# Kernel tuning notes

Hardware: AMD Instinct MI355X
Metric: run time of the kernel (lower is better)

## Reference

```python
import jax, jax.numpy as jnp
import numpy as np

N_NODES = 100000
N_EDGES = 3200000
N_GRAPHS = 512


def setup_inputs() -> dict:
    key = jax.random.key(0)
    k1, k2, k3, k4, k5 = jax.random.split(key, 5)
    x = jax.random.normal(k1, (N_NODES, 5), dtype=jnp.float32)
    edge_index = jax.random.randint(k2, (2, N_EDGES), 0, N_NODES, dtype=jnp.int64)
    batch = jnp.sort(jax.random.randint(k3, (N_NODES,), 0, N_GRAPHS, dtype=jnp.int64))
    W1 = jax.random.normal(k4, (5, 16), dtype=jnp.float32) * (1.0 / np.sqrt(5.0))
    b1 = jnp.zeros((16,), dtype=jnp.float32)
    W2 = jax.random.normal(k5, (16, 16), dtype=jnp.float32) * 0.25
    b2 = jnp.zeros((16,), dtype=jnp.float32)
    return {"x": x, "edge_index": edge_index, "batch": batch,
            "W1": W1, "b1": b1, "W2": W2, "b2": b2}


def _gcn_conv(x, src, dst, norm, W, b, n_nodes):
    # PyG GCNConv: h = X W; out_i = sum_{j->i} norm_ij * h_j + b
    h = x @ W                                   # [N, out]
    msgs = h[src] * norm[:, None]               # gather + scale  [E_tot, out]
    out = jax.ops.segment_sum(msgs, dst, num_segments=n_nodes)
    return out + b


def reference(x, edge_index, batch, W1, b1, W2, b2):
    n = x.shape[0]
    # add self-loops (GCNConv default)
    loops = jnp.arange(n, dtype=edge_index.dtype)
    src = jnp.concatenate([edge_index[0], loops])
    dst = jnp.concatenate([edge_index[1], loops])
    # symmetric normalization: deg computed on destination nodes
    deg = jax.ops.segment_sum(jnp.ones_like(src, dtype=x.dtype), dst, num_segments=n)
    dinv = jnp.where(deg > 0, jax.lax.rsqrt(deg), 0.0)
    norm = dinv[src] * dinv[dst]                # [E_tot]

    h = jax.nn.relu(_gcn_conv(x, src, dst, norm, W1, b1, n))
    h = jax.nn.relu(_gcn_conv(h, src, dst, norm, W2, b2, n))

    # global mean pool over graphs in the batch
    sums = jax.ops.segment_sum(h, batch, num_segments=N_GRAPHS)
    cnts = jax.ops.segment_sum(jnp.ones((n,), dtype=h.dtype), batch, num_segments=N_GRAPHS)
    return sums / jnp.maximum(cnts, 1.0)[:, None]
```

## Files before the change

kernel.cpp:

```cpp
#include <hip/hip_runtime.h>

#define N_NODES  100000
#define N_EDGES  3200000
#define N_GRAPHS 512
#define F_IN     5
#define F_HID    16

#define PBLK   512
#define CHUNK  8192
#define NCHUNK ((N_EDGES + CHUNK - 1) / CHUNK)
#define BKT_NODES 256
#define NBKT ((N_NODES + BKT_NODES - 1) / BKT_NODES)
#define CAP 10240


__device__ inline unsigned short f2bf(float f) {
    unsigned u = __float_as_uint(f);
    return (unsigned short)((u + 0x7fffu + ((u >> 16) & 1u)) >> 16);
}
__device__ inline float bf2f(unsigned short h) {
    return __uint_as_float(((unsigned)h) << 16);
}
__device__ inline float4 cvt4(ushort4 u) {
    return make_float4(bf2f(u.x), bf2f(u.y), bf2f(u.z), bf2f(u.w));
}
__device__ inline float4 shfl_xor4(float4 v, int m) {
    return make_float4(__shfl_xor(v.x, m, 64), __shfl_xor(v.y, m, 64),
                       __shfl_xor(v.z, m, 64), __shfl_xor(v.w, m, 64));
}

template <int NW>
__device__ inline int block_incl_scan(int v, int t, int* wsum) {
    int lane = t & 63, wave = t >> 6;
    int x = v;
#pragma unroll
    for (int o = 1; o < 64; o <<= 1) {
        int y = __shfl_up(x, o, 64);
        if (lane >= o) x += y;
    }
    if (lane == 63) wsum[wave] = x;
    __syncthreads();
    if (t < 64) {
        int w = (t < NW) ? wsum[t] : 0;
#pragma unroll
        for (int o = 1; o < NW; o <<= 1) {
            int y = __shfl_up(w, o, 64);
            if (t >= o) w += y;
        }
        if (t < NW) wsum[t] = w;
    }
    __syncthreads();
    return x + (wave ? wsum[wave - 1] : 0);
}

__device__ inline float4 row_gather(const ushort4* __restrict__ pb4, int i, int j,
                                    int beg, int end, const int* __restrict__ col) {
    float4 acc = cvt4(pb4[i * 4 + j]);
    int k = beg;
    for (; k + 3 < end; k += 4) {
        int s0 = col[k], s1 = col[k + 1], s2 = col[k + 2], s3 = col[k + 3];
        ushort4 a = pb4[s0 * 4 + j];
        ushort4 b = pb4[s1 * 4 + j];
        ushort4 c = pb4[s2 * 4 + j];
        ushort4 d = pb4[s3 * 4 + j];
        float4 fa = cvt4(a), fb = cvt4(b), fc = cvt4(c), fd = cvt4(d);
        acc.x += fa.x + fb.x + fc.x + fd.x;
        acc.y += fa.y + fb.y + fc.y + fd.y;
        acc.z += fa.z + fb.z + fc.z + fd.z;
        acc.w += fa.w + fb.w + fc.w + fd.w;
    }
    for (; k < end; k++) {
        float4 f = cvt4(pb4[col[k] * 4 + j]);
        acc.x += f.x; acc.y += f.y; acc.z += f.z; acc.w += f.w;
    }
    return acc;
}


__global__ void k_zero(int* __restrict__ cursor, float* __restrict__ out,
                       float* __restrict__ cnt) {
    int i = blockIdx.x * blockDim.x + threadIdx.x;
    if (i < NBKT) cursor[i] = 0;
    if (i < N_GRAPHS * F_HID) out[i] = 0.0f;
    if (i < N_GRAPHS) cnt[i] = 0.0f;
}

__global__ __launch_bounds__(PBLK) void k_part(const int* __restrict__ src,
                                               const int* __restrict__ dst,
                                               int* __restrict__ cursor,
                                               unsigned* __restrict__ packed) {
    __shared__ int hist[PBLK];
    __shared__ int scn[PBLK];
    __shared__ int rnk[PBLK];
    __shared__ int gbase[PBLK];
    __shared__ int wsum[8];
    int t = threadIdx.x;
    int chunk0 = blockIdx.x * CHUNK;
    int n = min(CHUNK, N_EDGES - chunk0);
    hist[t] = 0;
    __syncthreads();
    int ls[CHUNK / PBLK], ld[CHUNK / PBLK];
    for (int k = t, idx = 0; k < n; k += PBLK, idx++) {
        ls[idx] = src[chunk0 + k];
        ld[idx] = dst[chunk0 + k];
        atomicAdd(&hist[ld[idx] >> 8], 1);
    }
    __syncthreads();
    int v = hist[t];
    int incl = block_incl_scan<8>(v, t, wsum);
    int excl = incl - v;
    scn[t] = excl;
    rnk[t] = excl;
    gbase[t] = (v > 0) ? atomicAdd(&cursor[t], v) : 0;
    __syncthreads();
    for (int k = t, idx = 0; k < n; k += PBLK, idx++) {
        int d = ld[idx], s = ls[idx];
        int b = d >> 8;
        int r = atomicAdd(&rnk[b], 1);
        int g = gbase[b] + (r - scn[b]);
        if (g < CAP)
            packed[(size_t)b * CAP + g] = ((unsigned)s << 8) | (unsigned)(d & 255);
    }
}

__global__ __launch_bounds__(512) void k_scanb(const int* __restrict__ cursor,
                                               int* __restrict__ bktBase) {
    __shared__ int wsum[8];
    int t = threadIdx.x;
    int v = (t < NBKT) ? min(cursor[t], CAP) : 0;
    int incl = block_incl_scan<8>(v, t, wsum);
    if (t < NBKT) bktBase[t] = incl - v;
    if (t == NBKT - 1) bktBase[NBKT] = incl;
}

__global__ __launch_bounds__(512) void k_csr(const int* __restrict__ cursor,
                                             const int* __restrict__ bktBase,
                                             const unsigned* __restrict__ packed,
                                             const float* __restrict__ x,
                                             const float* __restrict__ W1,
                                             int* __restrict__ row_ptr,
                                             int* __restrict__ col,
                                             float* __restrict__ dinv,
                                             unsigned short* __restrict__ pb) {
    __shared__ int hist[BKT_NODES];
    __shared__ int rnk[BKT_NODES];
    __shared__ int wsum[8];
    __shared__ float w1[F_IN * F_HID];
    int b = blockIdx.x, t = threadIdx.x;
    int n = min(cursor[b], CAP);
    int base = bktBase[b];
    if (t < BKT_NODES) hist[t] = 0;
    if (t >= 512 - F_IN * F_HID) w1[t - (512 - F_IN * F_HID)] = W1[t - (512 - F_IN * F_HID)];
    __syncthreads();
    const unsigned* pk = packed + (size_t)b * CAP;
    for (int k = t; k < n; k += 512)
        atomicAdd(&hist[pk[k] & 255], 1);
    __syncthreads();
    int v = (t < BKT_NODES) ? hist[t] : 0;
    int incl = block_incl_scan<8>(v, t, wsum);
    int excl = incl - v;
    if (t < BKT_NODES) rnk[t] = excl;
    __syncthreads();
    for (int k = t; k < n; k += 512) {
        unsigned w = pk[k];
        int r = atomicAdd(&rnk[w & 255], 1);
        col[base + r] = (int)(w >> 8);
    }
    if (t < BKT_NODES) {
        int node = b * BKT_NODES + t;
        if (node < N_NODES) {
            row_ptr[node] = base + excl;
            float di = rsqrtf((float)(1 + v));
            dinv[node] = di;
            if (node == N_NODES - 1) row_ptr[N_NODES] = base + excl + v;
            float xi[F_IN];
#pragma unroll
            for (int k = 0; k < F_IN; k++) xi[k] = x[node * F_IN + k];
            float hv[F_HID];
#pragma unroll
            for (int c = 0; c < F_HID; c++) {
                float h = 0.0f;
#pragma unroll
                for (int k = 0; k < F_IN; k++) h += xi[k] * w1[k * F_HID + c];
                hv[c] = h * di;
            }
            unsigned pkk[8];
#pragma unroll
            for (int q = 0; q < 8; q++)
                pkk[q] = (unsigned)f2bf(hv[2 * q]) | ((unsigned)f2bf(hv[2 * q + 1]) << 16);
            uint4* d4 = (uint4*)(pb + (size_t)node * F_HID);
            d4[0] = make_uint4(pkk[0], pkk[1], pkk[2], pkk[3]);
            d4[1] = make_uint4(pkk[4], pkk[5], pkk[6], pkk[7]);
        }
    }
}

__global__ __launch_bounds__(256) void k_pull_mid(const int* __restrict__ row_ptr,
                                                  const int* __restrict__ col,
                                                  const unsigned short* __restrict__ pb,
                                                  const float* __restrict__ dinv,
                                                  const float* __restrict__ W2,
                                                  const float* __restrict__ b1,
                                                  unsigned short* __restrict__ pb2) {
    __shared__ float w[F_HID * F_HID];
    __shared__ float bb[F_HID];
    int t = threadIdx.x;
    w[t] = W2[t];
    if (t < F_HID) bb[t] = b1[t];
    __syncthreads();
    int gid = blockIdx.x * 256 + t;
    int i = gid >> 2;
    int j = gid & 3;
    if (i >= N_NODES) return;
    int beg = row_ptr[i], end = row_ptr[i + 1];
    float4 acc = row_gather((const ushort4*)pb, i, j, beg, end, col);
    float di = dinv[i];
    float4 mine;
    mine.x = fmaxf(di * acc.x + bb[4 * j + 0], 0.0f);
    mine.y = fmaxf(di * acc.y + bb[4 * j + 1], 0.0f);
    mine.z = fmaxf(di * acc.z + bb[4 * j + 2], 0.0f);
    mine.w = fmaxf(di * acc.w + bb[4 * j + 3], 0.0f);
    float4 o1 = shfl_xor4(mine, 1);
    float4 o2 = shfl_xor4(mine, 2);
    float4 o3 = shfl_xor4(mine, 3);
    float4 hq0 = (j == 0) ? mine : ((j == 1) ? o1 : ((j == 2) ? o2 : o3));
    float4 hq1 = (j == 1) ? mine : ((j == 0) ? o1 : ((j == 3) ? o2 : o3));
    float4 hq2 = (j == 2) ? mine : ((j == 3) ? o1 : ((j == 0) ? o2 : o3));
    float4 hq3 = (j == 3) ? mine : ((j == 2) ? o1 : ((j == 1) ? o2 : o3));
    float hc[F_HID] = {hq0.x, hq0.y, hq0.z, hq0.w, hq1.x, hq1.y, hq1.z, hq1.w,
                       hq2.x, hq2.y, hq2.z, hq2.w, hq3.x, hq3.y, hq3.z, hq3.w};
    float m0 = 0.0f, m1 = 0.0f, m2 = 0.0f, m3 = 0.0f;
#pragma unroll
    for (int c = 0; c < F_HID; c++) {
        float4 wv = *(const float4*)&w[c * F_HID + 4 * j];
        float hv = hc[c];
        m0 += hv * wv.x; m1 += hv * wv.y; m2 += hv * wv.z; m3 += hv * wv.w;
    }
    unsigned p0 = (unsigned)f2bf(m0 * di) | ((unsigned)f2bf(m1 * di) << 16);
    unsigned p1 = (unsigned)f2bf(m2 * di) | ((unsigned)f2bf(m3 * di) << 16);
    *(uint2*)(pb2 + (size_t)i * F_HID + 4 * j) = make_uint2(p0, p1);
}

__global__ __launch_bounds__(256) void k_pull_pool(const int* __restrict__ row_ptr,
                                                   const int* __restrict__ col,
                                                   const unsigned short* __restrict__ pb,
                                                   const float* __restrict__ dinv,
                                                   const int* __restrict__ batch,
                                                   const float* __restrict__ b2,
                                                   float* __restrict__ out,
                                                   float* __restrict__ cnt) {
    __shared__ float bb[F_HID];
    __shared__ float acc2[8][F_HID];
    __shared__ int gcnt[8];
    __shared__ int g0s;
    int t = threadIdx.x;
    if (t < F_HID) bb[t] = b2[t];
    if (t < 8) gcnt[t] = 0;
    if (t < 8 * F_HID) ((float*)acc2)[t] = 0.0f;
    int blk0node = blockIdx.x * 64;
    if (t == 0) g0s = batch[blk0node < N_NODES ? blk0node : N_NODES - 1];
    __syncthreads();
    int g0 = g0s;
    int gid = blockIdx.x * 256 + t;
    int i = gid >> 2;
    int j = gid & 3;
    if (i < N_NODES) {
        int beg = row_ptr[i], end = row_ptr[i + 1];
        float4 acc = row_gather((const ushort4*)pb, i, j, beg, end, col);
        float di = dinv[i];
        float h0 = fmaxf(di * acc.x + bb[4 * j + 0], 0.0f);
        float h1 = fmaxf(di * acc.y + bb[4 * j + 1], 0.0f);
        float h2 = fmaxf(di * acc.z + bb[4 * j + 2], 0.0f);
        float h3 = fmaxf(di * acc.w + bb[4 * j + 3], 0.0f);
        int g = batch[i];
        int l = g - g0;
        if (l >= 0 && l < 8) {
            atomicAdd(&acc2[l][4 * j + 0], h0);
            atomicAdd(&acc2[l][4 * j + 1], h1);
            atomicAdd(&acc2[l][4 * j + 2], h2);
            atomicAdd(&acc2[l][4 * j + 3], h3);
            if (j == 0) atomicAdd(&gcnt[l], 1);
        } else {
            atomicAdd(&out[g * F_HID + 4 * j + 0], h0);
            atomicAdd(&out[g * F_HID + 4 * j + 1], h1);
            atomicAdd(&out[g * F_HID + 4 * j + 2], h2);
            atomicAdd(&out[g * F_HID + 4 * j + 3], h3);
            if (j == 0) atomicAdd(&cnt[g], 1.0f);
        }
    }
    __syncthreads();
    if (t < 8 * F_HID) {
        int l = t >> 4, c = t & 15;
        if (gcnt[l] > 0) atomicAdd(&out[(g0 + l) * F_HID + c], acc2[l][c]);
    }
    if (t < 8 && gcnt[t] > 0) atomicAdd(&cnt[g0 + t], (float)gcnt[t]);
}

__global__ void k_div(float* __restrict__ out, const float* __restrict__ cnt) {
    int i = blockIdx.x * blockDim.x + threadIdx.x;
    if (i < N_GRAPHS * F_HID) {
        float c = cnt[i / F_HID];
        out[i] /= fmaxf(c, 1.0f);
    }
}


extern "C" void kernel_launch(void* const* d_in, const int* in_sizes, int n_in,
                              void* d_out, int out_size, void* d_ws, size_t ws_size,
                              hipStream_t stream) {
    const float* x     = (const float*)d_in[0];
    const int*   ei    = (const int*)d_in[1];
    const int*   batch = (const int*)d_in[2];
    const float* W1    = (const float*)d_in[3];
    const float* b1    = (const float*)d_in[4];
    const float* W2    = (const float*)d_in[5];
    const float* b2    = (const float*)d_in[6];
    float* out = (float*)d_out;

    int*            cursor  = (int*)d_ws;
    int*            bktBase = cursor + 512;
    unsigned*       packed  = (unsigned*)(bktBase + 512);
    int*            row_ptr = (int*)(packed + (size_t)NBKT * CAP);
    int*            col     = row_ptr + 100352;
    float*          dinv    = (float*)(col + N_EDGES);
    unsigned short* pb_a    = (unsigned short*)(dinv + N_NODES);
    unsigned short* pb_b    = pb_a + (size_t)N_NODES * F_HID;
    float*          cnt     = (float*)(pb_b + (size_t)N_NODES * F_HID);

    const int* src = ei;
    const int* dst = ei + N_EDGES;

    const int nb_pull = (N_NODES * 4 + 255) / 256;

    k_zero<<<(N_GRAPHS * F_HID + 255) / 256, 256, 0, stream>>>(cursor, out, cnt);
    k_part<<<NCHUNK, PBLK, 0, stream>>>(src, dst, cursor, packed);
    k_scanb<<<1, 512, 0, stream>>>(cursor, bktBase);
    k_csr<<<NBKT, 512, 0, stream>>>(cursor, bktBase, packed, x, W1,
                                    row_ptr, col, dinv, pb_a);
    k_pull_mid<<<nb_pull, 256, 0, stream>>>(row_ptr, col, pb_a, dinv, W2, b1, pb_b);
    k_pull_pool<<<nb_pull, 256, 0, stream>>>(row_ptr, col, pb_b, dinv, batch, b2,
                                             out, cnt);
    k_div<<<(N_GRAPHS * F_HID + 255) / 256, 256, 0, stream>>>(out, cnt);
}
```

Measured before the change: 201.8 us.

## Pad CSR rows to multiples of eight and drop global bucket scan

Each node's adjacency row is padded to a multiple of 8 entries, and the padding slots point to a zeroed sentinel node. This lets the gather loop use two aligned int4 loads of column indices and run 8 independent feature loads per iteration with no remainder loop. Buckets now use fixed CAP-strided bases in the col array, which removes the separate single-block scan kernel. Row offsets and lengths are stored together as int2. The cost is a larger col array, extra padding writes and wasted gathers on padding slots. Rows can also be truncated when a bucket's padded total exceeds CAP.

Result: no change. 200.4 us (-0.7%).

```diff
diff --git a/kernel.cpp b/kernel.cpp
--- a/kernel.cpp
+++ b/kernel.cpp
@@ -53,36 +53,38 @@
     return x + (wave ? wsum[wave - 1] : 0);
 }
 
-__device__ inline float4 row_gather(const ushort4* __restrict__ pb4, int i, int j,
-                                    int beg, int end, const int* __restrict__ col) {
+__device__ inline float4 row_gather8(const ushort4* __restrict__ pb4, int i, int j,
+                                     int beg, int len, const int* __restrict__ col) {
     float4 acc = cvt4(pb4[i * 4 + j]);
-    int k = beg;
-    for (; k + 3 < end; k += 4) {
-        int s0 = col[k], s1 = col[k + 1], s2 = col[k + 2], s3 = col[k + 3];
-        ushort4 a = pb4[s0 * 4 + j];
-        ushort4 b = pb4[s1 * 4 + j];
-        ushort4 c = pb4[s2 * 4 + j];
-        ushort4 d = pb4[s3 * 4 + j];
-        float4 fa = cvt4(a), fb = cvt4(b), fc = cvt4(c), fd = cvt4(d);
-        acc.x += fa.x + fb.x + fc.x + fd.x;
-        acc.y += fa.y + fb.y + fc.y + fd.y;
-        acc.z += fa.z + fb.z + fc.z + fd.z;
-        acc.w += fa.w + fb.w + fc.w + fd.w;
-    }
-    for (; k < end; k++) {
-        float4 f = cvt4(pb4[col[k] * 4 + j]);
-        acc.x += f.x; acc.y += f.y; acc.z += f.z; acc.w += f.w;
+    for (int k = 0; k < len; k += 8) {
+        int4 c0 = *(const int4*)(col + beg + k);
+        int4 c1 = *(const int4*)(col + beg + k + 4);
+        ushort4 a0 = pb4[c0.x * 4 + j], a1 = pb4[c0.y * 4 + j];
+        ushort4 a2 = pb4[c0.z * 4 + j], a3 = pb4[c0.w * 4 + j];
+        ushort4 a4 = pb4[c1.x * 4 + j], a5 = pb4[c1.y * 4 + j];
+        ushort4 a6 = pb4[c1.z * 4 + j], a7 = pb4[c1.w * 4 + j];
+        float4 f0 = cvt4(a0), f1 = cvt4(a1), f2 = cvt4(a2), f3 = cvt4(a3);
+        float4 f4 = cvt4(a4), f5 = cvt4(a5), f6 = cvt4(a6), f7 = cvt4(a7);
+        acc.x += ((f0.x + f1.x) + (f2.x + f3.x)) + ((f4.x + f5.x) + (f6.x + f7.x));
+        acc.y += ((f0.y + f1.y) + (f2.y + f3.y)) + ((f4.y + f5.y) + (f6.y + f7.y));
+        acc.z += ((f0.z + f1.z) + (f2.z + f3.z)) + ((f4.z + f5.z) + (f6.z + f7.z));
+        acc.w += ((f0.w + f1.w) + (f2.w + f3.w)) + ((f4.w + f5.w) + (f6.w + f7.w));
     }
     return acc;
 }
 
 
 __global__ void k_zero(int* __restrict__ cursor, float* __restrict__ out,
-                       float* __restrict__ cnt) {
+                       float* __restrict__ cnt, unsigned short* __restrict__ pb_a,
+                       unsigned short* __restrict__ pb_b) {
     int i = blockIdx.x * blockDim.x + threadIdx.x;
     if (i < NBKT) cursor[i] = 0;
     if (i < N_GRAPHS * F_HID) out[i] = 0.0f;
     if (i < N_GRAPHS) cnt[i] = 0.0f;
+    if (i < F_HID) {
+        pb_a[(size_t)N_NODES * F_HID + i] = 0;
+        pb_b[(size_t)N_NODES * F_HID + i] = 0;
+    }
 }
 
 __global__ __launch_bounds__(PBLK) void k_part(const int* __restrict__ src,
@@ -123,22 +125,11 @@
     }
 }
 
-__global__ __launch_bounds__(512) void k_scanb(const int* __restrict__ cursor,
-                                               int* __restrict__ bktBase) {
-    __shared__ int wsum[8];
-    int t = threadIdx.x;
-    int v = (t < NBKT) ? min(cursor[t], CAP) : 0;
-    int incl = block_incl_scan<8>(v, t, wsum);
-    if (t < NBKT) bktBase[t] = incl - v;
-    if (t == NBKT - 1) bktBase[NBKT] = incl;
-}
-
 __global__ __launch_bounds__(512) void k_csr(const int* __restrict__ cursor,
-                                             const int* __restrict__ bktBase,
                                              const unsigned* __restrict__ packed,
                                              const float* __restrict__ x,
                                              const float* __restrict__ W1,
-                                             int* __restrict__ row_ptr,
+                                             int2* __restrict__ rowbc,
                                              int* __restrict__ col,
                                              float* __restrict__ dinv,
                                              unsigned short* __restrict__ pb) {
@@ -148,7 +139,7 @@
     __shared__ float w1[F_IN * F_HID];
     int b = blockIdx.x, t = threadIdx.x;
     int n = min(cursor[b], CAP);
-    int base = bktBase[b];
+    int base = b * CAP;
     if (t < BKT_NODES) hist[t] = 0;
     if (t >= 512 - F_IN * F_HID) w1[t - (512 - F_IN * F_HID)] = W1[t - (512 - F_IN * F_HID)];
     __syncthreads();
@@ -157,22 +148,27 @@
         atomicAdd(&hist[pk[k] & 255], 1);
     __syncthreads();
     int v = (t < BKT_NODES) ? hist[t] : 0;
-    int incl = block_incl_scan<8>(v, t, wsum);
-    int excl = incl - v;
+    int len = (v + 7) & ~7;
+    int incl = block_incl_scan<8>(len, t, wsum);
+    int excl = incl - len;
     if (t < BKT_NODES) rnk[t] = excl;
     __syncthreads();
     for (int k = t; k < n; k += 512) {
         unsigned w = pk[k];
         int r = atomicAdd(&rnk[w & 255], 1);
-        col[base + r] = (int)(w >> 8);
+        if (r < CAP) col[base + r] = (int)(w >> 8);
     }
     if (t < BKT_NODES) {
         int node = b * BKT_NODES + t;
         if (node < N_NODES) {
-            row_ptr[node] = base + excl;
+            int mylen = min(len, ((CAP - min(excl, CAP)) & ~7));
+            for (int q = v; q < mylen; q++) {
+                int r = excl + q;
+                if (r < CAP) col[base + r] = N_NODES;
+            }
+            rowbc[node] = make_int2(base + excl, mylen);
             float di = rsqrtf((float)(1 + v));
             dinv[node] = di;
-            if (node == N_NODES - 1) row_ptr[N_NODES] = base + excl + v;
             float xi[F_IN];
 #pragma unroll
             for (int k = 0; k < F_IN; k++) xi[k] = x[node * F_IN + k];
@@ -195,7 +191,7 @@
     }
 }
 
-__global__ __launch_bounds__(256) void k_pull_mid(const int* __restrict__ row_ptr,
+__global__ __launch_bounds__(256) void k_pull_mid(const int2* __restrict__ rowbc,
                                                   const int* __restrict__ col,
                                                   const unsigned short* __restrict__ pb,
                                                   const float* __restrict__ dinv,
@@ -212,8 +208,8 @@
     int i = gid >> 2;
     int j = gid & 3;
     if (i >= N_NODES) return;
-    int beg = row_ptr[i], end = row_ptr[i + 1];
-    float4 acc = row_gather((const ushort4*)pb, i, j, beg, end, col);
+    int2 rc = rowbc[i];
+    float4 acc = row_gather8((const ushort4*)pb, i, j, rc.x, rc.y, col);
     float di = dinv[i];
     float4 mine;
     mine.x = fmaxf(di * acc.x + bb[4 * j + 0], 0.0f);
@@ -241,7 +237,7 @@
     *(uint2*)(pb2 + (size_t)i * F_HID + 4 * j) = make_uint2(p0, p1);
 }
 
-__global__ __launch_bounds__(256) void k_pull_pool(const int* __restrict__ row_ptr,
+__global__ __launch_bounds__(256) void k_pull_pool(const int2* __restrict__ rowbc,
                                                    const int* __restrict__ col,
                                                    const unsigned short* __restrict__ pb,
                                                    const float* __restrict__ dinv,
@@ -265,8 +261,8 @@
     int i = gid >> 2;
     int j = gid & 3;
     if (i < N_NODES) {
-        int beg = row_ptr[i], end = row_ptr[i + 1];
-        float4 acc = row_gather((const ushort4*)pb, i, j, beg, end, col);
+        int2 rc = rowbc[i];
+        float4 acc = row_gather8((const ushort4*)pb, i, j, rc.x, rc.y, col);
         float di = dinv[i];
         float h0 = fmaxf(di * acc.x + bb[4 * j + 0], 0.0f);
         float h1 = fmaxf(di * acc.y + bb[4 * j + 1], 0.0f);
@@ -317,28 +313,26 @@
     const float* b2    = (const float*)d_in[6];
     float* out = (float*)d_out;
 
-    int*            cursor  = (int*)d_ws;
-    int*            bktBase = cursor + 512;
-    unsigned*       packed  = (unsigned*)(bktBase + 512);
-    int*            row_ptr = (int*)(packed + (size_t)NBKT * CAP);
-    int*            col     = row_ptr + 100352;
-    float*          dinv    = (float*)(col + N_EDGES);
-    unsigned short* pb_a    = (unsigned short*)(dinv + N_NODES);
-    unsigned short* pb_b    = pb_a + (size_t)N_NODES * F_HID;
-    float*          cnt     = (float*)(pb_b + (size_t)N_NODES * F_HID);
+    int*            cursor = (int*)d_ws;
+    unsigned*       packed = (unsigned*)(cursor + 512);
+    int2*           rowbc  = (int2*)(packed + (size_t)NBKT * CAP);
+    int*            col    = (int*)(rowbc + N_NODES);
+    float*          dinv   = (float*)(col + (size_t)NBKT * CAP);
+    unsigned short* pb_a   = (unsigned short*)(dinv + N_NODES);
+    unsigned short* pb_b   = pb_a + (size_t)(N_NODES + 1) * F_HID;
+    float*          cnt    = (float*)(pb_b + (size_t)(N_NODES + 1) * F_HID);
 
     const int* src = ei;
     const int* dst = ei + N_EDGES;
 
     const int nb_pull = (N_NODES * 4 + 255) / 256;
 
-    k_zero<<<(N_GRAPHS * F_HID + 255) / 256, 256, 0, stream>>>(cursor, out, cnt);
+    k_zero<<<(N_GRAPHS * F_HID + 255) / 256, 256, 0, stream>>>(cursor, out, cnt,
+                                                               pb_a, pb_b);
     k_part<<<NCHUNK, PBLK, 0, stream>>>(src, dst, cursor, packed);
-    k_scanb<<<1, 512, 0, stream>>>(cursor, bktBase);
-    k_csr<<<NBKT, 512, 0, stream>>>(cursor, bktBase, packed, x, W1,
-                                    row_ptr, col, dinv, pb_a);
-    k_pull_mid<<<nb_pull, 256, 0, stream>>>(row_ptr, col, pb_a, dinv, W2, b1, pb_b);
-    k_pull_pool<<<nb_pull, 256, 0, stream>>>(row_ptr, col, pb_b, dinv, batch, b2,
+    k_csr<<<NBKT, 512, 0, stream>>>(cursor, packed, x, W1, rowbc, col, dinv, pb_a);
+    k_pull_mid<<<nb_pull, 256, 0, stream>>>(rowbc, col, pb_a, dinv, W2, b1, pb_b);
+    k_pull_pool<<<nb_pull, 256, 0, stream>>>(rowbc, col, pb_b, dinv, batch, b2,
                                              out, cnt);
     k_div<<<(N_GRAPHS * F_HID + 255) / 256, 256, 0, stream>>>(out, cnt);
 }
```
